# Optimization experiments

Hardware: AMD Instinct MI355X
Metric: run time of the kernel (lower is better)

The kernel has to match this reference:

```python
import jax, jax.numpy as jnp
import numpy as np

D_MODEL = 1024
N_HEADS = 16
HEAD_DIM = D_MODEL // N_HEADS
ROPE_BASE = 10000.0
NEG_INF = -1.0e9


def rotate_half(x):
    # interleaved pairs: (-x2_i, x1_i) re-flattened to last dim
    x1 = x[..., ::2]
    x2 = x[..., 1::2]
    return jnp.stack((-x2, x1), axis=-1).reshape(x.shape)


def rope_sin_cos(seq_len, head_dim, dtype):
    inv_freq = 1.0 / (ROPE_BASE ** (jnp.arange(0, head_dim, 2, dtype=jnp.float32) / head_dim))
    t = jnp.arange(seq_len, dtype=jnp.float32)
    freqs = jnp.einsum('i,j->ij', t, inv_freq)          # [T, hd/2]
    emb = jnp.concatenate((freqs, freqs), axis=-1)       # [T, hd]
    return jnp.sin(emb).astype(dtype), jnp.cos(emb).astype(dtype)


def apply_rope(x, sin, cos):
    # x: [B, H, T, hd]; sin/cos: [T, hd]
    return x * cos[None, None] + rotate_half(x) * sin[None, None]


def setup_inputs() -> dict:
    key = jax.random.key(0)
    ks = jax.random.split(key, 9)
    B, T, D = 2, 2048, D_MODEL
    q = jax.random.normal(ks[0], (B, T, D), dtype=jnp.float32)
    k = jax.random.normal(ks[1], (B, T, D), dtype=jnp.float32)
    v = jax.random.normal(ks[2], (B, T, D), dtype=jnp.float32)
    # causal additive mask, broadcastable over [B, H, Tq, Tk]
    causal = jnp.triu(jnp.full((T, T), NEG_INF, dtype=jnp.float32), k=1)
    attn_mask = causal[None, None]
    key_padding_mask = jax.random.uniform(ks[3], (B, T)) < 0.05
    scale = 1.0 / np.sqrt(D)
    Wq = jax.random.normal(ks[4], (D, D), dtype=jnp.float32) * scale
    Wk = jax.random.normal(ks[5], (D, D), dtype=jnp.float32) * scale
    Wv = jax.random.normal(ks[6], (D, D), dtype=jnp.float32) * scale
    Wo = jax.random.normal(ks[7], (D, D), dtype=jnp.float32) * scale
    return {"q": q, "k": k, "v": v, "attn_mask": attn_mask,
            "key_padding_mask": key_padding_mask,
            "Wq": Wq, "Wk": Wk, "Wv": Wv, "Wo": Wo}


def reference(q, k, v, attn_mask, key_padding_mask, Wq, Wk, Wv, Wo):
    B, Tq, _ = q.shape
    Tk = k.shape[1]
    H, hd = N_HEADS, HEAD_DIM
    # projections (nn.Linear: x @ W.T), split heads -> [B, H, T, hd]
    qh = (q @ Wq.T).reshape(B, Tq, H, hd).transpose(0, 2, 1, 3)
    kh = (k @ Wk.T).reshape(B, Tk, H, hd).transpose(0, 2, 1, 3)
    vh = (v @ Wv.T).reshape(B, Tk, H, hd).transpose(0, 2, 1, 3)
    sin_q, cos_q = rope_sin_cos(Tq, hd, q.dtype)
    sin_k, cos_k = rope_sin_cos(Tk, hd, k.dtype)
    qh = apply_rope(qh, sin_q, cos_q)
    kh = apply_rope(kh, sin_k, cos_k)
    scores = jnp.einsum('bhqd,bhkd->bhqk', qh, kh) / np.sqrt(hd)
    scores = scores + attn_mask
    scores = jnp.where(key_padding_mask[:, None, None, :], NEG_INF, scores)
    attn = jax.nn.softmax(scores, axis=-1)
    out = jnp.einsum('bhqk,bhkd->bhqd', attn, vh)
    out = out.transpose(0, 2, 1, 3).reshape(B, Tq, H * hd)
    return out @ Wo.T
```

## Files before the change

kernel.cpp:

```cpp
#include <hip/hip_runtime.h>
#include <stdint.h>

typedef __bf16 bf16x8 __attribute__((ext_vector_type(8)));
typedef float f32x4 __attribute__((ext_vector_type(4)));
typedef float f32x16 __attribute__((ext_vector_type(16)));

#define NEG_BIG2 (-1.442695040e9f)
#define SC_LOG2  (0.180336880f)

__device__ __forceinline__ unsigned short f2b(float f) {
  union { float f; unsigned int u; } c; c.f = f;
  unsigned int u = c.u;
  u += 0x7FFFu + ((u >> 16) & 1u);
  return (unsigned short)(u >> 16);
}
__device__ __forceinline__ float b2f(unsigned short h) {
  union { unsigned int u; float f; } c; c.u = ((unsigned int)h) << 16;
  return c.f;
}
__device__ __forceinline__ unsigned int pk2(float a, float b) {
  __bf16 x = (__bf16)a, y = (__bf16)b;
  unsigned short xu, yu;
  __builtin_memcpy(&xu, &x, 2);
  __builtin_memcpy(&yu, &y, 2);
  return (unsigned)xu | ((unsigned)yu << 16);
}
__device__ __forceinline__ float ex2(float x) {
  float r; asm("v_exp_f32 %0, %1" : "=v"(r) : "v"(x)); return r;
}

typedef const __attribute__((address_space(1))) unsigned int ga_u32;
typedef __attribute__((address_space(3))) unsigned int ls_u32;
__device__ __forceinline__ void gld16(const void* g, void* l) {
  __builtin_amdgcn_global_load_lds((ga_u32*)g, (ls_u32*)l, 16, 0, 0);
}

__device__ __forceinline__ void swap_pair(unsigned a, unsigned b, int hi,
                                          unsigned& lo_out, unsigned& hi_out) {
#if __has_builtin(__builtin_amdgcn_permlane32_swap)
  auto r = __builtin_amdgcn_permlane32_swap(a, b, false, false);
  lo_out = r[0]; hi_out = r[1];
#else
  unsigned pa = __shfl_xor(a, 32), pb = __shfl_xor(b, 32);
  lo_out = hi ? pb : a;
  hi_out = hi ? b : pa;
#endif
}

__global__ __launch_bounds__(256) void prep_k(
    const void* __restrict__ kpm,
    const float* __restrict__ Wq, const float* __restrict__ Wk,
    const float* __restrict__ Wv, const float* __restrict__ Wo,
    const float* __restrict__ q, const float* __restrict__ k,
    const float* __restrict__ v,
    unsigned long long* __restrict__ pmask,
    float* __restrict__ sin_t, float* __restrict__ cos_t,
    unsigned short* __restrict__ Wb,
    unsigned short* __restrict__ qb, unsigned short* __restrict__ kb,
    unsigned short* __restrict__ vb) {
  const int bid = blockIdx.x, tid = threadIdx.x;
  if (bid == 0) {
    __shared__ int flg;
    if (tid == 0) flg = 0;
    __syncthreads();
    unsigned int vv = 0;
    for (int i = tid; i < 1024; i += 256) vv |= ((const unsigned int*)kpm)[i];
    if (vv & ~1u) atomicOr(&flg, 1);
    __syncthreads();
    const int bytes = flg;
    const int w = tid >> 6, lane = tid & 63;
    for (int i = w; i < 64; i += 4) {
      int b = i >> 5, kbq = i & 31;
      int idx = b * 2048 + kbq * 64 + lane;
      int pad = bytes ? (int)((const unsigned char*)kpm)[idx] : ((const int*)kpm)[idx];
      unsigned long long pm = __ballot(pad != 0);
      if (lane == 0) pmask[i] = pm;
    }
  } else if (bid < 513) {
    int i = (bid - 1) * 256 + tid;
    int t = i >> 6, d = i & 63, f = d & 31;
    double inv = exp(-((double)(2 * f) / 64.0) * log(10000.0));
    double ang = (double)t * inv;
    sin_t[i] = (float)sin(ang);
    cos_t[i] = (float)cos(ang);
  } else if (bid < 2561) {
    size_t g = (size_t)(bid - 513) * 256 + tid;
    size_t i8 = g * 8;
    int t = (int)(i8 >> 20);
    const float* src = (t == 0 ? Wq : t == 1 ? Wk : t == 2 ? Wv : Wo) + (i8 & 1048575);
    float4 a = *(const float4*)src, c = *(const float4*)(src + 4);
    uint4 o = { pk2(a.x, a.y), pk2(a.z, a.w), pk2(c.x, c.y), pk2(c.z, c.w) };
    *(uint4*)&Wb[i8] = o;
  } else {
    size_t g = (size_t)(bid - 2561) * 256 + tid;
    size_t i8 = g * 8;
    int t = (int)(i8 >> 22);
    size_t off = i8 & 4194303;
    const float* src = (t == 0 ? q : t == 1 ? k : v) + off;
    unsigned short* dst = (t == 0 ? qb : t == 1 ? kb : vb) + off;
    float4 a = *(const float4*)src, c = *(const float4*)(src + 4);
    uint4 o = { pk2(a.x, a.y), pk2(a.z, a.w), pk2(c.x, c.y), pk2(c.z, c.w) };
    *(uint4*)dst = o;
  }
}

template<bool ABF>
__global__ __launch_bounds__(256) void qkv_k(const void* __restrict__ A0,
                                             const void* __restrict__ A1,
                                             const void* __restrict__ A2,
                                             const unsigned short* __restrict__ Wb,
                                             const float* __restrict__ sin_t,
                                             const float* __restrict__ cos_t,
                                             unsigned short* __restrict__ qh,
                                             unsigned short* __restrict__ kh,
                                             unsigned short* __restrict__ vt) {
  const int z = blockIdx.z;
  const void* Ap = (z == 0) ? A0 : (z == 1) ? A1 : A2;
  const unsigned short* Wp = Wb + (size_t)z * 1048576;
  unsigned short* outp = (z == 0) ? qh : (z == 1) ? kh : vt;

  __shared__ unsigned short As[2][128 * 32];
  __shared__ unsigned short Bs[2][128 * 32];
  const int M0 = blockIdx.x * 128, N0 = blockIdx.y * 128;
  const int tid = threadIdx.x, lane = tid & 63, w = tid >> 6;
  const int wr = w >> 1, wc = w & 1;
  const int lrow = lane & 15, lgrp = lane >> 4;

  const f32x4 Z4 = {0.f, 0.f, 0.f, 0.f};
  f32x4 acc[4][4];
#pragma unroll
  for (int i = 0; i < 4; ++i)
#pragma unroll
    for (int j = 0; j < 4; ++j) acc[i][j] = Z4;

  auto STAGE = [&](int bu, int kt) {
    if (ABF) {
      const unsigned short* Ab = (const unsigned short*)Ap;
#pragma unroll
      for (int i = 0; i < 2; ++i) {
        const unsigned short* gA = Ab +
            (size_t)(M0 + i * 64 + w * 16 + (lane >> 2)) * 1024 + kt + (lane & 3) * 8;
        gld16(gA, &As[bu][i * 2048 + w * 512]);
      }
    } else {
      const int row = tid >> 1, half = tid & 1;
      const float* ap = (const float*)Ap + (size_t)(M0 + row) * 1024 + kt + half * 16;
      float4 f0 = *(const float4*)ap, f1 = *(const float4*)(ap + 4);
      float4 f2 = *(const float4*)(ap + 8), f3 = *(const float4*)(ap + 12);
      uint4 u0 = { pk2(f0.x, f0.y), pk2(f0.z, f0.w), pk2(f1.x, f1.y), pk2(f1.z, f1.w) };
      uint4 u1 = { pk2(f2.x, f2.y), pk2(f2.z, f2.w), pk2(f3.x, f3.y), pk2(f3.z, f3.w) };
      *(uint4*)&As[bu][row * 32 + half * 16] = u0;
      *(uint4*)&As[bu][row * 32 + half * 16 + 8] = u1;
    }
#pragma unroll
    for (int i = 0; i < 2; ++i) {
      const unsigned short* gB = Wp +
          (size_t)(N0 + i * 64 + w * 16 + (lane >> 2)) * 1024 + kt + (lane & 3) * 8;
      gld16(gB, &Bs[bu][i * 2048 + w * 512]);
    }
  };

  STAGE(0, 0);
  int cur = 0;
  for (int kt = 0; kt < 1024; kt += 32) {
    __syncthreads();
    if (kt + 32 < 1024) STAGE(cur ^ 1, kt + 32);
    bf16x8 af[4], bfv[4];
#pragma unroll
    for (int m = 0; m < 4; ++m)
      af[m] = *(const bf16x8*)&As[cur][(wr * 64 + m * 16 + lrow) * 32 + lgrp * 8];
#pragma unroll
    for (int n = 0; n < 4; ++n)
      bfv[n] = *(const bf16x8*)&Bs[cur][(wc * 64 + n * 16 + lrow) * 32 + lgrp * 8];
    __builtin_amdgcn_s_setprio(1);
#pragma unroll
    for (int m = 0; m < 4; ++m)
#pragma unroll
      for (int n = 0; n < 4; ++n)
        acc[m][n] = __builtin_amdgcn_mfma_f32_16x16x32_bf16(af[m], bfv[n], acc[m][n], 0, 0, 0);
    __builtin_amdgcn_s_setprio(0);
    cur ^= 1;
  }

#pragma unroll
  for (int mi = 0; mi < 4; ++mi)
#pragma unroll
    for (int ni = 0; ni < 4; ++ni) {
      const int m = M0 + wr * 64 + mi * 16 + lgrp * 4;
      const int n = N0 + wc * 64 + ni * 16 + lrow;
      const int b = m >> 11, t = m & 2047;
      const int d = n & 63;
      if (z < 2) {
        const float sc = (z == 0) ? SC_LOG2 : 1.0f;
        unsigned short* o = outp +
            ((size_t)(b * 16 + (n >> 6)) * 2048 + t) * 64 + d;
#pragma unroll
        for (int r = 0; r < 4; ++r) {
          const float xv = acc[mi][ni][r];
          const float pr = __shfl_xor(xv, 1);
          const int tt = t + r;
          const float cs = cos_t[tt * 64 + d];
          const float sn = sin_t[tt * 64 + d];
          const float ov = (xv * cs + ((d & 1) ? pr : -pr) * sn) * sc;
          o[(size_t)r * 64] = f2b(ov);
        }
      } else {
        unsigned short* o = outp +
            ((size_t)(b * 16 + (n >> 6)) * 64 + d) * 2048 + t;
        *(ushort4*)o = make_ushort4(f2b(acc[mi][ni][0]), f2b(acc[mi][ni][1]),
                                    f2b(acc[mi][ni][2]), f2b(acc[mi][ni][3]));
      }
    }
}

__global__ __launch_bounds__(256) void gemm_o_k(const unsigned short* __restrict__ Ab,
                                                const unsigned short* __restrict__ Wp,
                                                float* __restrict__ outp) {
  __shared__ unsigned short As[2][64 * 32];
  __shared__ unsigned short Bs[2][128 * 32];
  const int M0 = blockIdx.x * 64, N0 = blockIdx.y * 128;
  const int tid = threadIdx.x, lane = tid & 63, w = tid >> 6;
  const int wr = w >> 1, wc = w & 1;
  const int lrow = lane & 15, lgrp = lane >> 4;

  const f32x4 Z4 = {0.f, 0.f, 0.f, 0.f};
  f32x4 acc[2][4];
#pragma unroll
  for (int i = 0; i < 2; ++i)
#pragma unroll
    for (int j = 0; j < 4; ++j) acc[i][j] = Z4;

  auto STAGE = [&](int bu, int kt) {
    {
      const unsigned short* gA = Ab +
          (size_t)(M0 + w * 16 + (lane >> 2)) * 1024 + kt + (lane & 3) * 8;
      gld16(gA, &As[bu][w * 512]);
    }
#pragma unroll
    for (int i = 0; i < 2; ++i) {
      const unsigned short* gB = Wp +
          (size_t)(N0 + i * 64 + w * 16 + (lane >> 2)) * 1024 + kt + (lane & 3) * 8;
      gld16(gB, &Bs[bu][i * 2048 + w * 512]);
    }
  };

  STAGE(0, 0);
  int cur = 0;
  for (int kt = 0; kt < 1024; kt += 32) {
    __syncthreads();
    if (kt + 32 < 1024) STAGE(cur ^ 1, kt + 32);
    bf16x8 af[2], bfv[4];
#pragma unroll
    for (int m = 0; m < 2; ++m)
      af[m] = *(const bf16x8*)&As[cur][(wr * 32 + m * 16 + lrow) * 32 + lgrp * 8];
#pragma unroll
    for (int n = 0; n < 4; ++n)
      bfv[n] = *(const bf16x8*)&Bs[cur][(wc * 64 + n * 16 + lrow) * 32 + lgrp * 8];
    __builtin_amdgcn_s_setprio(1);
#pragma unroll
    for (int m = 0; m < 2; ++m)
#pragma unroll
      for (int n = 0; n < 4; ++n)
        acc[m][n] = __builtin_amdgcn_mfma_f32_16x16x32_bf16(af[m], bfv[n], acc[m][n], 0, 0, 0);
    __builtin_amdgcn_s_setprio(0);
    cur ^= 1;
  }

#pragma unroll
  for (int mi = 0; mi < 2; ++mi)
#pragma unroll
    for (int ni = 0; ni < 4; ++ni) {
      const int m = M0 + wr * 32 + mi * 16 + lgrp * 4;
      const int n = N0 + wc * 64 + ni * 16 + lrow;
      float* o = outp + (size_t)m * 1024 + n;
#pragma unroll
      for (int r = 0; r < 4; ++r) o[(size_t)r * 1024] = acc[mi][ni][r];
    }
}

__global__ __launch_bounds__(256, 2) void attn_k(
    const unsigned short* __restrict__ qh, const unsigned short* __restrict__ kh,
    const unsigned short* __restrict__ vt, const unsigned long long* __restrict__ pmask,
    unsigned short* __restrict__ ao) {
  const int bid = blockIdx.x;
  const int x = bid & 7, j = bid >> 3;
  const int bh = x * 4 + (j & 3);
  const int jj = j >> 2;
  const int tile = (j < 32) ? (15 - jj) : (jj - 8);
  const int b = bh >> 4, h = bh & 15;
  const int tid = threadIdx.x, lane = tid & 63, w = tid >> 6;
  const int ln31 = lane & 31, hi = lane >> 5;

  __shared__ char Kb[2][8192];
  __shared__ char Vb[2][8192];
  __shared__ int flagv;

  const size_t bh_off = (size_t)bh * 2048 * 64;
  const int qw = tile * 128 + w * 32;
  const int q_abs = qw + ln31;
  const int nkv_w = qw / 64 + 1;
  const int nkv_b = tile * 2 + 2;
  const int swz = (ln31 & 7) << 4;

  bf16x8 qf[4];
#pragma unroll
  for (int dc = 0; dc < 4; ++dc)
    qf[dc] = *(const bf16x8*)(qh + bh_off + (size_t)(qw + ln31) * 64 + dc * 16 + hi * 8);

  const f32x16 Z16 = {0.f,0.f,0.f,0.f,0.f,0.f,0.f,0.f,0.f,0.f,0.f,0.f,0.f,0.f,0.f,0.f};
  f32x16 O0 = Z16, O1 = Z16;
  float m_run = -INFINITY, l_run = 0.f;

  uint4 kr0, kr1, vr0, vr1;
  const int srow = tid >> 2, sseg = tid & 3;
  const int sbase = srow * 128 + sseg * 32;
  const int sswz = (srow & 7) << 4;

  auto stage_load = [&](int kbi) {
    const unsigned short* kp = kh + bh_off + (size_t)(kbi * 64 + srow) * 64 + sseg * 16;
    kr0 = *(const uint4*)kp; kr1 = *(const uint4*)(kp + 8);
    const unsigned short* vp = vt + bh_off + (size_t)srow * 2048 + kbi * 64 + sseg * 16;
    vr0 = *(const uint4*)vp; vr1 = *(const uint4*)(vp + 8);
  };
  auto stage_write = [&](int bu) {
    *(uint4*)(Kb[bu] + (sbase ^ sswz)) = kr0;
    *(uint4*)(Kb[bu] + ((sbase + 16) ^ sswz)) = kr1;
    *(uint4*)(Vb[bu] + (sbase ^ sswz)) = vr0;
    *(uint4*)(Vb[bu] + ((sbase + 16) ^ sswz)) = vr1;
  };

  auto compute = [&](int kb, int cur) {
    const unsigned long long pmh = pmask[b * 32 + kb] >> (hi * 4);
    f32x16 S0 = Z16, S1 = Z16;
    __builtin_amdgcn_s_setprio(1);
#pragma unroll
    for (int dc = 0; dc < 4; ++dc) {
      bf16x8 k0 = *(const bf16x8*)(Kb[cur] + ((ln31 * 128 + dc * 32 + hi * 16) ^ swz));
      bf16x8 k1 = *(const bf16x8*)(Kb[cur] + (((ln31 + 32) * 128 + dc * 32 + hi * 16) ^ swz));
      S0 = __builtin_amdgcn_mfma_f32_32x32x16_bf16(k0, qf[dc], S0, 0, 0, 0);
      S1 = __builtin_amdgcn_mfma_f32_32x32x16_bf16(k1, qf[dc], S1, 0, 0, 0);
    }
    __builtin_amdgcn_s_setprio(0);

    const bool diag = (kb * 64 + 63) > qw;
    if (diag) {
#pragma unroll
      for (int r = 0; r < 16; ++r) {
        const int kloc = (r & 3) + 8 * (r >> 2);
        float sv = S0[r];
        sv = ((pmh >> kloc) & 1) ? NEG_BIG2
             : ((kb * 64 + kloc + 4 * hi > q_abs) ? sv + NEG_BIG2 : sv);
        S0[r] = sv;
        float sw = S1[r];
        sw = ((pmh >> (kloc + 32)) & 1) ? NEG_BIG2
             : ((kb * 64 + 32 + kloc + 4 * hi > q_abs) ? sw + NEG_BIG2 : sw);
        S1[r] = sw;
      }
    } else {
#pragma unroll
      for (int r = 0; r < 16; ++r) {
        const int kloc = (r & 3) + 8 * (r >> 2);
        S0[r] = ((pmh >> kloc) & 1) ? NEG_BIG2 : S0[r];
        S1[r] = ((pmh >> (kloc + 32)) & 1) ? NEG_BIG2 : S1[r];
      }
    }

    float vm = fmaxf(S0[0], S0[1]);
#pragma unroll
    for (int r = 2; r < 16; r += 2) vm = fmaxf(vm, fmaxf(S0[r], S0[r + 1]));
#pragma unroll
    for (int r = 0; r < 16; r += 2) vm = fmaxf(vm, fmaxf(S1[r], S1[r + 1]));
    vm = fmaxf(vm, __shfl_xor(vm, 32));

    if (__any(vm > m_run + 11.5f)) {
      const float mnew = fmaxf(m_run, vm);
      const float alpha = ex2(m_run - mnew);
      m_run = mnew;
      l_run *= alpha;
      O0 *= alpha; O1 *= alpha;
    }
    float rs = 0.f;
#pragma unroll
    for (int r = 0; r < 16; ++r) { float p = ex2(S0[r] - m_run); S0[r] = p; rs += p; }
#pragma unroll
    for (int r = 0; r < 16; ++r) { float p = ex2(S1[r] - m_run); S1[r] = p; rs += p; }
    rs += __shfl_xor(rs, 32);
    l_run += rs;

    union U8 { uint4 u; bf16x8 v; };
    bf16x8 pa[4];
#pragma unroll
    for (int kt = 0; kt < 2; ++kt) {
#pragma unroll
      for (int hf = 0; hf < 2; ++hf) {
        float p0, p1, p2, p3, p4, p5, p6, p7;
        if (kt == 0) {
          if (hf == 0) { p0=S0[0];p1=S0[1];p2=S0[2];p3=S0[3];p4=S0[4];p5=S0[5];p6=S0[6];p7=S0[7]; }
          else         { p0=S0[8];p1=S0[9];p2=S0[10];p3=S0[11];p4=S0[12];p5=S0[13];p6=S0[14];p7=S0[15]; }
        } else {
          if (hf == 0) { p0=S1[0];p1=S1[1];p2=S1[2];p3=S1[3];p4=S1[4];p5=S1[5];p6=S1[6];p7=S1[7]; }
          else         { p0=S1[8];p1=S1[9];p2=S1[10];p3=S1[11];p4=S1[12];p5=S1[13];p6=S1[14];p7=S1[15]; }
        }
        unsigned e0 = pk2(p0, p1), e1 = pk2(p2, p3);
        unsigned o0 = pk2(p4, p5), o1 = pk2(p6, p7);
        unsigned a0, b0_, a1, b1_;
        swap_pair(e0, o0, hi, a0, b0_);
        swap_pair(e1, o1, hi, a1, b1_);
        U8 u; u.u = make_uint4(a0, a1, b0_, b1_);
        pa[kt * 2 + hf] = u.v;
      }
    }

    __builtin_amdgcn_s_setprio(1);
#pragma unroll
    for (int c = 0; c < 4; ++c) {
      bf16x8 v0 = *(const bf16x8*)(Vb[cur] + ((ln31 * 128 + c * 32 + hi * 16) ^ swz));
      bf16x8 v1 = *(const bf16x8*)(Vb[cur] + (((ln31 + 32) * 128 + c * 32 + hi * 16) ^ swz));
      O0 = __builtin_amdgcn_mfma_f32_32x32x16_bf16(v0, pa[c], O0, 0, 0, 0);
      O1 = __builtin_amdgcn_mfma_f32_32x32x16_bf16(v1, pa[c], O1, 0, 0, 0);
    }
    __builtin_amdgcn_s_setprio(0);
  };

  stage_load(0);
  stage_write(0);
  for (int kb = 0; kb < nkv_b; ++kb) {
    if (kb + 1 < nkv_b) stage_load(kb + 1);
    __syncthreads();
    if (kb < nkv_w) compute(kb, kb & 1);
    if (kb + 1 < nkv_b) stage_write((kb + 1) & 1);
  }

  if (tid == 0) flagv = 0;
  __syncthreads();
  if (m_run <= -7.2e8f) flagv = 1;
  __syncthreads();
  if (flagv) {
    for (int kb = nkv_b - 1; kb < 32; ++kb) {
      if (kb + 1 < 32) stage_load(kb + 1);
      __syncthreads();
      if (kb >= nkv_w) compute(kb, kb & 1);
      if (kb + 1 < 32) stage_write((kb + 1) & 1);
    }
  }

  {
    const float inv = 1.0f / l_run;
    unsigned short* op = ao + (size_t)(b * 2048 + qw + ln31) * 1024 + h * 64;
#pragma unroll
    for (int g2 = 0; g2 < 4; ++g2) {
      const int d0 = 8 * g2 + 4 * hi;
      *(ushort4*)(op + d0) = make_ushort4(
          f2b(O0[g2 * 4 + 0] * inv), f2b(O0[g2 * 4 + 1] * inv),
          f2b(O0[g2 * 4 + 2] * inv), f2b(O0[g2 * 4 + 3] * inv));
      *(ushort4*)(op + 32 + d0) = make_ushort4(
          f2b(O1[g2 * 4 + 0] * inv), f2b(O1[g2 * 4 + 1] * inv),
          f2b(O1[g2 * 4 + 2] * inv), f2b(O1[g2 * 4 + 3] * inv));
    }
  }
}

extern "C" void kernel_launch(void* const* d_in, const int* in_sizes, int n_in,
                              void* d_out, int out_size, void* d_ws, size_t ws_size,
                              hipStream_t stream) {
  const float* q  = (const float*)d_in[0];
  const float* k  = (const float*)d_in[1];
  const float* v  = (const float*)d_in[2];
  const void*  kpm = d_in[4];
  const float* Wq = (const float*)d_in[5];
  const float* Wk = (const float*)d_in[6];
  const float* Wv = (const float*)d_in[7];
  const float* Wo = (const float*)d_in[8];

  char* ws = (char*)d_ws;
  unsigned short* qh = (unsigned short*)(ws);
  unsigned short* kh = (unsigned short*)(ws + (8u << 20));
  unsigned short* vt = (unsigned short*)(ws + (16u << 20));
  unsigned short* ao = (unsigned short*)(ws + (24u << 20));
  unsigned short* Wb = (unsigned short*)(ws + (32u << 20));
  float* sin_t = (float*)(ws + (40u << 20));
  float* cos_t = (float*)(ws + (40u << 20) + 524288);
  unsigned long long* pmask = (unsigned long long*)(ws + (41u << 20));
  unsigned short* qb = (unsigned short*)(ws + (42u << 20));
  unsigned short* kb = (unsigned short*)(ws + (50u << 20));
  unsigned short* vb = (unsigned short*)(ws + (58u << 20));

  const bool big = ws_size >= (66ull << 20);

  prep_k<<<big ? 8705 : 2561, 256, 0, stream>>>(
      kpm, Wq, Wk, Wv, Wo, q, k, v, pmask, sin_t, cos_t, Wb, qb, kb, vb);

  dim3 gq(32, 8, 3);
  if (big) {
    qkv_k<true><<<gq, 256, 0, stream>>>(qb, kb, vb, Wb, sin_t, cos_t, qh, kh, vt);
  } else {
    qkv_k<false><<<gq, 256, 0, stream>>>(q, k, v, Wb, sin_t, cos_t, qh, kh, vt);
  }

  attn_k<<<512, 256, 0, stream>>>(qh, kh, vt, pmask, ao);

  gemm_o_k<<<dim3(64, 8), 256, 0, stream>>>(ao, Wb + 3145728, (float*)d_out);
}
```

Measured before the change: 129.5 us.

## Store K/V in pre-swizzled tiles and stage attention loads directly into LDS

```diff
diff --git a/kernel.cpp b/kernel.cpp
--- a/kernel.cpp
+++ b/kernel.cpp
@@ -190,8 +190,7 @@
       const int n = N0 + wc * 64 + ni * 16 + lrow;
       const int b = m >> 11, t = m & 2047;
       const int d = n & 63;
-      if (z < 2) {
-        const float sc = (z == 0) ? SC_LOG2 : 1.0f;
+      if (z == 0) {
         unsigned short* o = outp +
             ((size_t)(b * 16 + (n >> 6)) * 2048 + t) * 64 + d;
 #pragma unroll
@@ -201,12 +200,25 @@
           const int tt = t + r;
           const float cs = cos_t[tt * 64 + d];
           const float sn = sin_t[tt * 64 + d];
-          const float ov = (xv * cs + ((d & 1) ? pr : -pr) * sn) * sc;
+          const float ov = (xv * cs + ((d & 1) ? pr : -pr) * sn) * SC_LOG2;
           o[(size_t)r * 64] = f2b(ov);
         }
+      } else if (z == 1) {
+        unsigned short* ob = outp + (size_t)(b * 16 + (n >> 6)) * 131072 + (t >> 6) * 4096;
+#pragma unroll
+        for (int r = 0; r < 4; ++r) {
+          const float xv = acc[mi][ni][r];
+          const float pr = __shfl_xor(xv, 1);
+          const int tt = t + r;
+          const float cs = cos_t[tt * 64 + d];
+          const float sn = sin_t[tt * 64 + d];
+          const float ov = xv * cs + ((d & 1) ? pr : -pr) * sn;
+          ob[(tt & 63) * 64 + (d ^ ((tt & 7) << 3))] = f2b(ov);
+        }
       } else {
-        unsigned short* o = outp +
-            ((size_t)(b * 16 + (n >> 6)) * 64 + d) * 2048 + t;
+        const int kl = t & 63;
+        unsigned short* o = outp + (size_t)(b * 16 + (n >> 6)) * 131072 + (t >> 6) * 4096
+                          + d * 64 + (kl ^ ((d & 7) << 3));
         *(ushort4*)o = make_ushort4(f2b(acc[mi][ni][0]), f2b(acc[mi][ni][1]),
                                     f2b(acc[mi][ni][2]), f2b(acc[mi][ni][3]));
       }
@@ -295,7 +307,7 @@
   __shared__ char Vb[2][8192];
   __shared__ int flagv;
 
-  const size_t bh_off = (size_t)bh * 2048 * 64;
+  const size_t bh_off = (size_t)bh * 131072;
   const int qw = tile * 128 + w * 32;
   const int q_abs = qw + ln31;
   const int nkv_w = qw / 64 + 1;
@@ -311,22 +323,15 @@
   f32x16 O0 = Z16, O1 = Z16;
   float m_run = -INFINITY, l_run = 0.f;
 
-  uint4 kr0, kr1, vr0, vr1;
-  const int srow = tid >> 2, sseg = tid & 3;
-  const int sbase = srow * 128 + sseg * 32;
-  const int sswz = (srow & 7) << 4;
-
-  auto stage_load = [&](int kbi) {
-    const unsigned short* kp = kh + bh_off + (size_t)(kbi * 64 + srow) * 64 + sseg * 16;
-    kr0 = *(const uint4*)kp; kr1 = *(const uint4*)(kp + 8);
-    const unsigned short* vp = vt + bh_off + (size_t)srow * 2048 + kbi * 64 + sseg * 16;
-    vr0 = *(const uint4*)vp; vr1 = *(const uint4*)(vp + 8);
-  };
-  auto stage_write = [&](int bu) {
-    *(uint4*)(Kb[bu] + (sbase ^ sswz)) = kr0;
-    *(uint4*)(Kb[bu] + ((sbase + 16) ^ sswz)) = kr1;
-    *(uint4*)(Vb[bu] + (sbase ^ sswz)) = vr0;
-    *(uint4*)(Vb[bu] + ((sbase + 16) ^ sswz)) = vr1;
+  auto stage = [&](int kbi, int bu) {
+    const unsigned short* kp = kh + bh_off + (size_t)kbi * 4096 + w * 512 + lane * 8;
+    char* kd = Kb[bu] + w * 1024;
+    gld16(kp, kd);
+    gld16(kp + 2048, kd + 4096);
+    const unsigned short* vp = vt + bh_off + (size_t)kbi * 4096 + w * 512 + lane * 8;
+    char* vd = Vb[bu] + w * 1024;
+    gld16(vp, vd);
+    gld16(vp + 2048, vd + 4096);
   };
 
   auto compute = [&](int kb, int cur) {
@@ -422,13 +427,11 @@
     __builtin_amdgcn_s_setprio(0);
   };
 
-  stage_load(0);
-  stage_write(0);
+  stage(0, 0);
   for (int kb = 0; kb < nkv_b; ++kb) {
-    if (kb + 1 < nkv_b) stage_load(kb + 1);
     __syncthreads();
+    if (kb + 1 < nkv_b) stage(kb + 1, (kb + 1) & 1);
     if (kb < nkv_w) compute(kb, kb & 1);
-    if (kb + 1 < nkv_b) stage_write((kb + 1) & 1);
   }
 
   if (tid == 0) flagv = 0;
@@ -437,10 +440,9 @@
   __syncthreads();
   if (flagv) {
     for (int kb = nkv_b - 1; kb < 32; ++kb) {
-      if (kb + 1 < 32) stage_load(kb + 1);
+      if (kb + 1 < 32) stage(kb + 1, (kb + 1) & 1);
       __syncthreads();
       if (kb >= nkv_w) compute(kb, kb & 1);
-      if (kb + 1 < 32) stage_write((kb + 1) & 1);
     }
   }
 
```

Result: no change. 131.0 us (+1.2%).
